# Performance work log

Hardware: AMD Instinct MI355X
Metric: run time of the kernel (lower is better)

## Reference

```python
import jax, jax.numpy as jnp
import numpy as np

H = 12      # num_heads
EPS = 1e-5  # LayerNorm eps (torch default)


def _ln(x, g, b):
    m = x.mean(-1, keepdims=True)
    v = x.var(-1, keepdims=True)
    return (x - m) * jax.lax.rsqrt(v + EPS) * g + b


def _rot_half(x):
    x1, x2 = x[..., 0::2], x[..., 1::2]
    return jnp.stack((-x2, x1), axis=-1).reshape(x.shape)


def _rope_tables(n, head_dim):
    # rotary-embedding-torch: RotaryEmbedding(dim=head_dim//2, use_xpos=True),
    # theta=10000, scale_base=512. Only first rot=head_dim//2 dims are rotated.
    rot = head_dim // 2
    inv = 1.0 / (10000.0 ** (jnp.arange(0, rot, 2, dtype=jnp.float32) / rot))
    t = jnp.arange(n, dtype=jnp.float32)
    freqs = jnp.repeat(t[:, None] * inv[None, :], 2, axis=-1)  # (n, rot), interleaved
    base = (jnp.arange(0, rot, 2, dtype=jnp.float32) + 0.4 * rot) / (1.4 * rot)
    power = (t - n // 2) / 512.0
    sc = base[None, :] ** power[:, None]
    sc = jnp.concatenate([sc, sc], axis=-1)  # (n, rot), concatenated (library behavior)
    return jnp.cos(freqs), jnp.sin(freqs), sc


def _attn_path(xn, Wqkv, bqkv, Wproj, bproj, qg, qb, kg, kb, R, rg, rb):
    B, N, D = xn.shape
    d = D // H
    qkv = xn @ Wqkv + bqkv
    q, k, v = jnp.split(qkv, 3, axis=-1)
    hd = lambda t: t.reshape(B, N, H, d).transpose(0, 2, 1, 3)  # (B,H,N,d)
    q, k, v = hd(q), hd(k), hd(v)
    q = _ln(q, qg, qb)  # per-head QK LayerNorm
    k = _ln(k, kg, kb)
    cos, sin, sc = _rope_tables(N, d)
    rot = d // 2

    def rope(t, s):  # rotate only first rot dims
        tl, tr = t[..., :rot], t[..., rot:]
        tl = tl * cos * s + _rot_half(tl) * sin * s
        return jnp.concatenate([tl, tr], axis=-1)

    q = rope(q, sc)
    v = rope(v, 1.0 / sc)  # source applies rope to (q, v), not k

    scores = jnp.einsum('bhid,bhjd->bhij', q, k) / jnp.sqrt(jnp.asarray(d, xn.dtype))
    p = jax.nn.softmax(scores, axis=-1)
    # SDPA(q,k,ones_NN)[...,i,j] == sum_k p[...,i,k] for every j (constant over j).
    # All downstream ops (head-mix einsum, LayerNorm over heads, @ v) therefore
    # reduce exactly to the per-(b,i) computation below, avoiding an N^3 matmul.
    s = p.sum(-1)                              # (B,H,N)
    mix = jnp.einsum('bhi,hg->big', s, R)      # (B,N,H)
    w = _ln(mix, rg, rb)                       # reattn LayerNorm over head axis
    vsum = v.sum(axis=2)                       # (B,H,d); (w @ v) with w const over j
    y = jnp.einsum('big,bgd->bigd', w, vsum).reshape(B, N, D)
    return y @ Wproj + bproj


def _cgmlp(xn, W1, b1, gg, gb, cw, cb, W2, b2):
    h = jax.nn.gelu(xn @ W1 + b1, approximate=False)
    c2 = h.shape[-1] // 2
    xr, xg = h[..., :c2], h[..., c2:]
    xg = _ln(xg, gg, gb).transpose(0, 2, 1)  # (B,C,T)
    K = cw.shape[-1]
    xg = jax.lax.conv_general_dilated(xg, cw, (1,), [((K - 1) // 2, (K - 1) // 2)],
                                      dimension_numbers=('NCH', 'OIH', 'NCH'),
                                      feature_group_count=c2)  # depthwise conv1d
    xg = (xg + cb[None, :, None]).transpose(0, 2, 1)
    return (xr * xg) @ W2 + b2


def reference(x, Wqkv, bqkv, Wproj, bproj, qn_g, qn_b, kn_g, kn_b, reattn_w, rn_g, rn_b,
              ln1_g, ln1_b, ln2_g, ln2_b, ls1, ls2, W1, b1, gn_g, gn_b, conv_w, conv_b,
              W2, b2, Wout, bout):
    # eval mode: dropout / drop_path are identity
    xa = _ln(x, ln1_g, ln1_b)
    attn = sum(_attn_path(xa, Wqkv[p], bqkv[p], Wproj[p], bproj[p], qn_g[p], qn_b[p],
                          kn_g[p], kn_b[p], reattn_w[p], rn_g[p], rn_b[p])
               for p in range(2))
    x_attn = x + ls1 * attn
    xm = _ln(x, ln2_g, ln2_b)
    x_mlp = x + ls2 * _cgmlp(xm, W1, b1, gn_g, gn_b, conv_w, conv_b, W2, b2)
    xf = jnp.concatenate([x_attn, x_mlp], axis=-1)
    return xf @ Wout + bout + x


def setup_inputs():
    B, N, D, P = 4, 1024, 768, 2
    d = D // H
    C = 4 * D
    c2 = C // 2
    K = 21
    ks = iter(jax.random.split(jax.random.key(0), 16))
    nrm = lambda s, sd=0.02: jax.random.normal(next(ks), s, jnp.float32) * sd
    return {
        'x': jax.random.normal(next(ks), (B, N, D), jnp.float32),
        'Wqkv': nrm((P, D, 3 * D)), 'bqkv': jnp.zeros((P, 3 * D)),
        'Wproj': nrm((P, D, D)), 'bproj': jnp.zeros((P, D)),
        'qn_g': jnp.ones((P, d)), 'qn_b': jnp.zeros((P, d)),
        'kn_g': jnp.ones((P, d)), 'kn_b': jnp.zeros((P, d)),
        'reattn_w': jax.random.normal(next(ks), (P, H, H), jnp.float32),
        'rn_g': jnp.ones((P, H)), 'rn_b': jnp.zeros((P, H)),
        'ln1_g': jnp.ones((D,)), 'ln1_b': jnp.zeros((D,)),
        'ln2_g': jnp.ones((D,)), 'ln2_b': jnp.zeros((D,)),
        'ls1': jnp.full((D,), 0.01, jnp.float32), 'ls2': jnp.full((D,), 0.01, jnp.float32),
        'W1': nrm((D, C)), 'b1': jnp.zeros((C,)),
        'gn_g': jnp.ones((c2,)), 'gn_b': jnp.zeros((c2,)),
        'conv_w': nrm((c2, 1, K), 0.1), 'conv_b': jnp.zeros((c2,)),
        'W2': nrm((c2, D)), 'b2': jnp.zeros((D,)),
        'Wout': nrm((2 * D, D)), 'bout': jnp.zeros((D,)),
    }
```

## Files before the change

### kernel.cpp

```cpp
#include <hip/hip_runtime.h>
#include <hip/hip_bf16.h>

typedef short s16x8 __attribute__((ext_vector_type(8)));
typedef float f32x4 __attribute__((ext_vector_type(4)));

#define C2 1536

__device__ __forceinline__ float b2f(ushort u){ return __uint_as_float(((unsigned)u)<<16); }
__device__ __forceinline__ ushort f2b(float f){ unsigned u = __float_as_uint(f); return (ushort)((u + 0x7fffu + ((u>>16)&1u)) >> 16); }

template<int EPI>
__global__ __launch_bounds__(256) void gemm_bf16(
    const ushort* __restrict__ A, const ushort* __restrict__ BT,
    int M, int N, int K,
    const float* __restrict__ bias, const float* __restrict__ scale,
    const float* __restrict__ xres,
    ushort* __restrict__ o16, ushort* __restrict__ o16b, float* __restrict__ o32)
{
    __shared__ ushort Al[128*32];
    __shared__ ushort Bl[128*32];
    const int t = threadIdx.x;
    const int m0 = blockIdx.y*128, n0 = blockIdx.x*128;
    const int lane = t & 63, wv = t >> 6;
    const int wm = (wv>>1)*64, wn = (wv&1)*64;
    const int r0 = lane & 15, q = lane >> 4;

    const int c0i = t, c1i = t + 256;
    const int lrow0 = ((c0i>>6)<<4) | (c0i&15), lkc0 = ((c0i>>4)&3) << 3;
    const int lrow1 = ((c1i>>6)<<4) | (c1i&15), lkc1 = ((c1i>>4)&3) << 3;
    const ushort* gA0 = A  + (size_t)(m0+lrow0)*K + lkc0;
    const ushort* gB0 = BT + (size_t)(n0+lrow0)*K + lkc0;
    const ushort* gA1 = A  + (size_t)(m0+lrow1)*K + lkc1;
    const ushort* gB1 = BT + (size_t)(n0+lrow1)*K + lkc1;

    f32x4 acc[4][4];
    #pragma unroll
    for (int i=0;i<4;++i)
        #pragma unroll
        for (int j=0;j<4;++j) acc[i][j] = (f32x4){0.f,0.f,0.f,0.f};

    const int nkt = K >> 5;
    uint4 ra0 = *(const uint4*)gA0;
    uint4 rb0 = *(const uint4*)gB0;
    uint4 ra1 = *(const uint4*)gA1;
    uint4 rb1 = *(const uint4*)gB1;
    for (int kt = 0; kt < nkt; ++kt) {
        __syncthreads();
        *(uint4*)&Al[c0i*8] = ra0;
        *(uint4*)&Bl[c0i*8] = rb0;
        *(uint4*)&Al[c1i*8] = ra1;
        *(uint4*)&Bl[c1i*8] = rb1;
        __syncthreads();
        if (kt+1 < nkt) {
            ra0 = *(const uint4*)(gA0 + (kt+1)*32);
            rb0 = *(const uint4*)(gB0 + (kt+1)*32);
            ra1 = *(const uint4*)(gA1 + (kt+1)*32);
            rb1 = *(const uint4*)(gB1 + (kt+1)*32);
        }
        s16x8 af[4], bfr[4];
        #pragma unroll
        for (int mt=0; mt<4; ++mt) af[mt]  = *(const s16x8*)&Al[(((wm>>4)+mt)*64 + lane)*8];
        #pragma unroll
        for (int nt=0; nt<4; ++nt) bfr[nt] = *(const s16x8*)&Bl[(((wn>>4)+nt)*64 + lane)*8];
        #pragma unroll
        for (int mt=0; mt<4; ++mt)
            #pragma unroll
            for (int nt=0; nt<4; ++nt)
                acc[mt][nt] = __builtin_amdgcn_mfma_f32_16x16x32_bf16(af[mt], bfr[nt], acc[mt][nt], 0,0,0);
    }

    #pragma unroll
    for (int mt=0; mt<4; ++mt) {
        #pragma unroll
        for (int nt=0; nt<4; ++nt) {
            int col = n0 + wn + nt*16 + r0;
            #pragma unroll
            for (int r=0; r<4; ++r) {
                int row = m0 + wm + mt*16 + q*4 + r;
                float v = acc[mt][nt][r];
                if (EPI == 0) {
                    o16[(size_t)row*N + col] = f2b(v + bias[col]);
                } else if (EPI == 1) {
                    v += bias[col];
                    float g = 0.5f*v*(1.0f + erff(v*0.70710678118f));
                    if (col < C2) o16 [(size_t)row*C2 + col]        = f2b(g);
                    else          o16b[(size_t)row*C2 + (col - C2)] = f2b(g);
                } else if (EPI == 2) {
                    v += bias[col];
                    o16[(size_t)row*1536 + 768 + col] = f2b(xres[(size_t)row*768 + col] + scale[col]*v);
                } else {
                    o32[(size_t)row*768 + col] = v + bias[col] + xres[(size_t)row*768 + col];
                }
            }
        }
    }
}

__global__ __launch_bounds__(256) void pack_bt(const float* __restrict__ src, ushort* __restrict__ dst,
                                               int K, int ld, int coff)
{
    __shared__ float tl[32*33];
    int kt = blockIdx.x*32, nt = blockIdx.y*32;
    int nl = threadIdx.x & 31, kg = threadIdx.x >> 5;
    #pragma unroll
    for (int kk=0; kk<4; ++kk) {
        int k = kg*4 + kk;
        tl[k*33 + nl] = src[(size_t)(kt + k)*ld + coff + nt + nl];
    }
    __syncthreads();
    int kcol = threadIdx.x & 31, ng = threadIdx.x >> 5;
    #pragma unroll
    for (int nn=0; nn<4; ++nn) {
        int nrow = ng*4 + nn;
        dst[(size_t)(nt + nrow)*K + kt + kcol] = f2b(tl[kcol*33 + nrow]);
    }
}

__global__ __launch_bounds__(256) void pack_bv(const float* __restrict__ bqkv, float* __restrict__ bvp)
{
    int idx = blockIdx.x*256 + threadIdx.x;
    if (idx < 1536) bvp[idx] = bqkv[(idx/768)*2304 + 1536 + (idx%768)];
}

__global__ __launch_bounds__(256) void ln_x_kernel(const float* __restrict__ x,
    const float* __restrict__ g1, const float* __restrict__ b1,
    const float* __restrict__ g2, const float* __restrict__ b2,
    ushort* __restrict__ xa, ushort* __restrict__ xm)
{
    __shared__ float sb[8];
    int row = blockIdx.x; int t = threadIdx.x;
    float v[3]; float s = 0.f, ss = 0.f;
    #pragma unroll
    for (int e=0; e<3; ++e) { v[e] = x[(size_t)row*768 + t + e*256]; s += v[e]; ss += v[e]*v[e]; }
    for (int o=32; o>0; o>>=1){ s += __shfl_down(s,o,64); ss += __shfl_down(ss,o,64); }
    int lane = t&63, w = t>>6;
    if (lane==0){ sb[w]=s; sb[4+w]=ss; }
    __syncthreads();
    s = sb[0]+sb[1]+sb[2]+sb[3]; ss = sb[4]+sb[5]+sb[6]+sb[7];
    float mean = s*(1.f/768.f);
    float var  = ss*(1.f/768.f) - mean*mean;
    float rstd = rsqrtf(var + 1e-5f);
    #pragma unroll
    for (int e=0; e<3; ++e){
        int c = t + e*256;
        float n = (v[e]-mean)*rstd;
        xa[(size_t)row*768 + c] = f2b(n*g1[c] + b1[c]);
        xm[(size_t)row*768 + c] = f2b(n*g2[c] + b2[c]);
    }
}

__global__ __launch_bounds__(256) void prep_kernel(
    float* __restrict__ w1t, float* __restrict__ w2t, float* __restrict__ wvec,
    float* __restrict__ attn_c, float* __restrict__ vsum,
    const float* __restrict__ R, const float* __restrict__ rng,
    const float* __restrict__ rnb, const float* __restrict__ bproj)
{
    int idx = blockIdx.x*256 + threadIdx.x;
    {
        int i = idx >> 6, j = idx & 63;
        float w1, w2;
        if (j < 32) {
            int m = j >> 1;
            float inv = powf(10000.f, -(float)m*(1.f/16.f));
            float fr = (float)i * inv;
            float c = cosf(fr), sn = sinf(fr);
            float power = ((float)i - 512.f) * (1.f/512.f);
            float basev = (2.f*(float)(j & 15) + 12.8f) * (1.f/44.8f);
            float sfac = powf(basev, -power);
            w1 = c * sfac;
            w2 = ((j & 1) ? sn : -sn) * sfac;
        } else { w1 = 1.f; w2 = 0.f; }
        w1t[idx] = w1; w2t[idx] = w2;
    }
    if (blockIdx.x >= 1 && blockIdx.x <= 12) {
        int k = (blockIdx.x-1)*256 + threadIdx.x;
        int o = k % 768;
        attn_c[k] = bproj[o] + bproj[768 + o];
    }
    if (blockIdx.x >= 13 && blockIdx.x <= 36) {
        int k = (blockIdx.x-13)*256 + threadIdx.x;
        vsum[k] = 0.f;
    }
    if (blockIdx.x == 0) {
        __shared__ float mixs[24];
        __shared__ float ws[24];
        int t = threadIdx.x;
        if (t < 24) {
            int p = t / 12, g = t % 12;
            float m = 0.f;
            for (int h=0; h<12; ++h) m += R[p*144 + h*12 + g];
            mixs[t] = m;
        }
        __syncthreads();
        if (t < 2) {
            float mean=0.f, var=0.f;
            for (int g=0; g<12; ++g) mean += mixs[t*12+g];
            mean *= (1.f/12.f);
            for (int g=0; g<12; ++g){ float d = mixs[t*12+g]-mean; var += d*d; }
            var *= (1.f/12.f);
            float rstd = rsqrtf(var + 1e-5f);
            for (int g=0; g<12; ++g)
                ws[t*12+g] = (mixs[t*12+g]-mean)*rstd*rng[t*12+g] + rnb[t*12+g];
        }
        __syncthreads();
        if (t < 24) wvec[t] = ws[t];
    }
}

__global__ __launch_bounds__(256) void rope_reduce(const ushort* __restrict__ V,
    const float* __restrict__ w1t, const float* __restrict__ w2t, float* __restrict__ vsum)
{
    int col = blockIdx.x*256 + threadIdx.x;
    int b = blockIdx.y;
    int i0 = blockIdx.z * 256;
    int j = col & 63;
    float acc = 0.f;
    const ushort* vp = V + (size_t)(b*1024 + i0)*1536;
    #pragma unroll 4
    for (int i=0; i<256; ++i) {
        float v1 = b2f(vp[(size_t)i*1536 + col]);
        float v2 = b2f(vp[(size_t)i*1536 + (col^1)]);
        int ii = i0 + i;
        acc += w1t[ii*64 + j]*v1 + w2t[ii*64 + j]*v2;
    }
    atomicAdd(&vsum[b*1536 + col], acc);
}

__global__ __launch_bounds__(256) void attn_gemm(const float* __restrict__ vsum,
    const float* __restrict__ wvec, const float* __restrict__ Wproj, float* __restrict__ attn_c)
{
    int o  = blockIdx.x*256 + threadIdx.x;
    int c0 = blockIdx.y * 96;
    int b  = blockIdx.z;
    int p  = c0 / 768;
    float acc = 0.f;
    #pragma unroll 4
    for (int cc=0; cc<96; ++cc) {
        int c = c0 + cc;
        int cl = c - p*768;
        float y = wvec[p*12 + (cl>>6)] * vsum[b*1536 + c];
        acc += y * Wproj[(size_t)p*589824 + (size_t)cl*768 + o];
    }
    atomicAdd(&attn_c[b*768 + o], acc);
}

__global__ __launch_bounds__(256) void xf_left(const float* __restrict__ x, const float* __restrict__ ls1,
    const float* __restrict__ attn_c, ushort* __restrict__ xf)
{
    int col = blockIdx.x*256 + threadIdx.x;
    int row = blockIdx.y;
    xf[(size_t)row*1536 + col] = f2b(x[(size_t)row*768 + col] + ls1[col]*attn_c[(row>>10)*768 + col]);
}

__global__ __launch_bounds__(256) void ln_gate(const ushort* __restrict__ xg,
    const float* __restrict__ g, const float* __restrict__ bta, ushort* __restrict__ out)
{
    __shared__ float sb[8];
    int row = blockIdx.x, t = threadIdx.x;
    float v[6]; float s=0.f, ss=0.f;
    #pragma unroll
    for (int e=0;e<6;++e){ v[e] = b2f(xg[(size_t)row*1536 + t + e*256]); s+=v[e]; ss+=v[e]*v[e]; }
    for (int o=32; o>0; o>>=1){ s += __shfl_down(s,o,64); ss += __shfl_down(ss,o,64); }
    int lane = t&63, w = t>>6;
    if (lane==0){ sb[w]=s; sb[4+w]=ss; }
    __syncthreads();
    s = sb[0]+sb[1]+sb[2]+sb[3]; ss = sb[4]+sb[5]+sb[6]+sb[7];
    float mean = s*(1.f/1536.f);
    float var  = ss*(1.f/1536.f) - mean*mean;
    float rstd = rsqrtf(var + 1e-5f);
    #pragma unroll
    for (int e=0;e<6;++e){
        int c = t + e*256;
        out[(size_t)row*1536 + c] = f2b((v[e]-mean)*rstd*g[c] + bta[c]);
    }
}

#define CROWS 128
#define CIN   (CROWS + 20)
#define CSTR  72
__global__ __launch_bounds__(256) void conv_mul(const ushort* __restrict__ xgln,
    const float* __restrict__ cw, const float* __restrict__ cb,
    const ushort* __restrict__ xr, ushort* __restrict__ u)
{
    __shared__ ushort tile[CIN * CSTR];
    const int c0 = blockIdx.x * 64;
    const int i0 = blockIdx.y * CROWS;
    const int b  = blockIdx.z;
    const int t  = threadIdx.x;
    const size_t base = (size_t)b*1024*1536;

    #pragma unroll
    for (int it = 0; it < 5; ++it) {
        int idx = it*256 + t;
        if (idx < CIN*8) {
            int r  = idx >> 3;
            int cq = (idx & 7) * 8;
            int si = i0 + r - 10;
            uint4 val = make_uint4(0u,0u,0u,0u);
            if (si >= 0 && si < 1024)
                val = *(const uint4*)(xgln + base + (size_t)si*1536 + c0 + cq);
            *(uint4*)&tile[r*CSTR + cq] = val;
        }
    }
    __syncthreads();

    const int ch = t & 63;
    const int o0 = (t >> 6) * 32;
    const int c  = c0 + ch;

    float w[21];
    #pragma unroll
    for (int k=0; k<21; ++k) w[k] = cw[c*21 + k];
    const float bias = cb[c];

    float win[21];
    #pragma unroll
    for (int j=0; j<20; ++j) win[j] = b2f(tile[(o0+j)*CSTR + ch]);

    #pragma unroll
    for (int j=0; j<32; ++j) {
        win[(j+20)%21] = b2f(tile[(o0+j+20)*CSTR + ch]);
        float acc = bias;
        #pragma unroll
        for (int k=0; k<21; ++k) acc += win[(j+k)%21] * w[k];
        size_t off = base + (size_t)(i0+o0+j)*1536 + c;
        u[off] = f2b(b2f(xr[off]) * acc);
    }
}

extern "C" void kernel_launch(void* const* d_in, const int* in_sizes, int n_in,
                              void* d_out, int out_size, void* d_ws, size_t ws_size,
                              hipStream_t stream)
{
    const float* x     = (const float*)d_in[0];
    const float* Wqkv  = (const float*)d_in[1];
    const float* bqkv  = (const float*)d_in[2];
    const float* Wproj = (const float*)d_in[3];
    const float* bproj = (const float*)d_in[4];
    const float* Rw    = (const float*)d_in[9];
    const float* rng   = (const float*)d_in[10];
    const float* rnb   = (const float*)d_in[11];
    const float* ln1g  = (const float*)d_in[12];
    const float* ln1b  = (const float*)d_in[13];
    const float* ln2g  = (const float*)d_in[14];
    const float* ln2b  = (const float*)d_in[15];
    const float* ls1   = (const float*)d_in[16];
    const float* ls2   = (const float*)d_in[17];
    const float* W1    = (const float*)d_in[18];
    const float* b1    = (const float*)d_in[19];
    const float* gng   = (const float*)d_in[20];
    const float* gnb   = (const float*)d_in[21];
    const float* cw    = (const float*)d_in[22];
    const float* cb    = (const float*)d_in[23];
    const float* W2    = (const float*)d_in[24];
    const float* b2    = (const float*)d_in[25];
    const float* Wout  = (const float*)d_in[26];
    const float* bout  = (const float*)d_in[27];
    float* out = (float*)d_out;

    char* ws = (char*)d_ws;
    size_t off = 0;
    auto alloc = [&](size_t bytes)->char* {
        char* p = ws + off;
        off += (bytes + 255) & ~(size_t)255;
        return p;
    };
    ushort* WvT   = (ushort*)alloc(1536*768*2);
    ushort* W1T   = (ushort*)alloc(3072*768*2);
    ushort* W2T   = (ushort*)alloc(768*1536*2);
    ushort* WoutT = (ushort*)alloc(768*1536*2);
    float*  bvp   = (float*)alloc(1536*4);
    float*  w1t   = (float*)alloc(65536*4);
    float*  w2t   = (float*)alloc(65536*4);
    float*  wvec  = (float*)alloc(24*4);
    float*  attnc = (float*)alloc(3072*4);
    float*  vsum  = (float*)alloc(6144*4);
    ushort* xa16  = (ushort*)alloc(4096*768*2);
    ushort* xm16  = (ushort*)alloc(4096*768*2);
    ushort* V16   = (ushort*)alloc(4096*1536*2);
    ushort* xg16  = (ushort*)alloc(4096*1536*2);
    ushort* xf16  = (ushort*)alloc(4096*1536*2);
    ushort* xgln  = xa16;
    ushort* xr16  = V16;
    ushort* u16   = xg16;
    (void)ws_size; (void)n_in; (void)in_sizes; (void)out_size;

    for (int p = 0; p < 2; ++p)
        pack_bt<<<dim3(24, 24), 256, 0, stream>>>(Wqkv + (size_t)p*768*2304, WvT + (size_t)p*768*768,
                                                  768, 2304, 1536);
    pack_bt<<<dim3(24, 96), 256, 0, stream>>>(W1,   W1T,   768,  3072, 0);
    pack_bt<<<dim3(48, 24), 256, 0, stream>>>(W2,   W2T,   1536, 768,  0);
    pack_bt<<<dim3(48, 24), 256, 0, stream>>>(Wout, WoutT, 1536, 768,  0);
    pack_bv<<<dim3(6), 256, 0, stream>>>(bqkv, bvp);
    prep_kernel<<<dim3(256), 256, 0, stream>>>(w1t, w2t, wvec, attnc, vsum, Rw, rng, rnb, bproj);

    ln_x_kernel<<<dim3(4096), 256, 0, stream>>>(x, ln1g, ln1b, ln2g, ln2b, xa16, xm16);

    gemm_bf16<0><<<dim3(12, 32), 256, 0, stream>>>(xa16, WvT, 4096, 1536, 768,
                                                   bvp, nullptr, nullptr, V16, nullptr, nullptr);
    rope_reduce<<<dim3(6, 4, 4), 256, 0, stream>>>(V16, w1t, w2t, vsum);
    attn_gemm<<<dim3(3, 16, 4), 256, 0, stream>>>(vsum, wvec, Wproj, attnc);
    xf_left<<<dim3(3, 4096), 256, 0, stream>>>(x, ls1, attnc, xf16);

    gemm_bf16<1><<<dim3(24, 32), 256, 0, stream>>>(xm16, W1T, 4096, 3072, 768,
                                                   b1, nullptr, nullptr, xr16, xg16, nullptr);
    ln_gate<<<dim3(4096), 256, 0, stream>>>(xg16, gng, gnb, xgln);
    conv_mul<<<dim3(24, 8, 4), 256, 0, stream>>>(xgln, cw, cb, xr16, u16);
    gemm_bf16<2><<<dim3(6, 32), 256, 0, stream>>>(u16, W2T, 4096, 768, 1536,
                                                  b2, ls2, x, xf16, nullptr, nullptr);
    gemm_bf16<3><<<dim3(6, 32), 256, 0, stream>>>(xf16, WoutT, 4096, 768, 1536,
                                                  bout, nullptr, x, nullptr, nullptr, out);
}
```

Baseline: 384.3 us.

## Double-buffer GEMM LDS tiles with two-stage register prefetch

Converts the bf16 GEMM main loop to ping-pong LDS buffers, with global loads issued two k-tiles ahead. The aim is one barrier per iteration instead of two, and overlap of LDS stores with the MFMA work. The costs are double the shared memory, more registers, and register arrays indexed by kt&1, which may spill to scratch if the loop is not unrolled.

```diff
diff --git a/kernel.cpp b/kernel.cpp
--- a/kernel.cpp
+++ b/kernel.cpp
@@ -17,8 +17,8 @@
     const float* __restrict__ xres,
     ushort* __restrict__ o16, ushort* __restrict__ o16b, float* __restrict__ o32)
 {
-    __shared__ ushort Al[128*32];
-    __shared__ ushort Bl[128*32];
+    __shared__ ushort Al[2][128*32];
+    __shared__ ushort Bl[2][128*32];
     const int t = threadIdx.x;
     const int m0 = blockIdx.y*128, n0 = blockIdx.x*128;
     const int lane = t & 63, wv = t >> 6;
@@ -40,28 +40,36 @@
         for (int j=0;j<4;++j) acc[i][j] = (f32x4){0.f,0.f,0.f,0.f};
 
     const int nkt = K >> 5;
-    uint4 ra0 = *(const uint4*)gA0;
-    uint4 rb0 = *(const uint4*)gB0;
-    uint4 ra1 = *(const uint4*)gA1;
-    uint4 rb1 = *(const uint4*)gB1;
+    uint4 ra0[2], rb0[2], ra1[2], rb1[2];
+    ra0[0] = *(const uint4*)gA0;        rb0[0] = *(const uint4*)gB0;
+    ra1[0] = *(const uint4*)gA1;        rb1[0] = *(const uint4*)gB1;
+    ra0[1] = *(const uint4*)(gA0 + 32); rb0[1] = *(const uint4*)(gB0 + 32);
+    ra1[1] = *(const uint4*)(gA1 + 32); rb1[1] = *(const uint4*)(gB1 + 32);
+    *(uint4*)&Al[0][c0i*8] = ra0[0];
+    *(uint4*)&Bl[0][c0i*8] = rb0[0];
+    *(uint4*)&Al[0][c1i*8] = ra1[0];
+    *(uint4*)&Bl[0][c1i*8] = rb1[0];
+
     for (int kt = 0; kt < nkt; ++kt) {
         __syncthreads();
-        *(uint4*)&Al[c0i*8] = ra0;
-        *(uint4*)&Bl[c0i*8] = rb0;
-        *(uint4*)&Al[c1i*8] = ra1;
-        *(uint4*)&Bl[c1i*8] = rb1;
-        __syncthreads();
+        const int cur = kt & 1, nxt = cur ^ 1;
+        s16x8 af[4], bfr[4];
+        #pragma unroll
+        for (int mt=0; mt<4; ++mt) af[mt]  = *(const s16x8*)&Al[cur][(((wm>>4)+mt)*64 + lane)*8];
+        #pragma unroll
+        for (int nt=0; nt<4; ++nt) bfr[nt] = *(const s16x8*)&Bl[cur][(((wn>>4)+nt)*64 + lane)*8];
         if (kt+1 < nkt) {
-            ra0 = *(const uint4*)(gA0 + (kt+1)*32);
-            rb0 = *(const uint4*)(gB0 + (kt+1)*32);
-            ra1 = *(const uint4*)(gA1 + (kt+1)*32);
-            rb1 = *(const uint4*)(gB1 + (kt+1)*32);
-        }
-        s16x8 af[4], bfr[4];
-        #pragma unroll
-        for (int mt=0; mt<4; ++mt) af[mt]  = *(const s16x8*)&Al[(((wm>>4)+mt)*64 + lane)*8];
-        #pragma unroll
-        for (int nt=0; nt<4; ++nt) bfr[nt] = *(const s16x8*)&Bl[(((wn>>4)+nt)*64 + lane)*8];
+            *(uint4*)&Al[nxt][c0i*8] = ra0[nxt];
+            *(uint4*)&Bl[nxt][c0i*8] = rb0[nxt];
+            *(uint4*)&Al[nxt][c1i*8] = ra1[nxt];
+            *(uint4*)&Bl[nxt][c1i*8] = rb1[nxt];
+        }
+        if (kt+2 < nkt) {
+            ra0[cur] = *(const uint4*)(gA0 + (kt+2)*32);
+            rb0[cur] = *(const uint4*)(gB0 + (kt+2)*32);
+            ra1[cur] = *(const uint4*)(gA1 + (kt+2)*32);
+            rb1[cur] = *(const uint4*)(gB1 + (kt+2)*32);
+        }
         #pragma unroll
         for (int mt=0; mt<4; ++mt)
             #pragma unroll
```

Result: slower. 544.8 us (+41.8%).
